# Kernel tuning notes

Measured on AMD Instinct MI355X. Metric: run time of the kernel, lower is better.

The kernel has to match this reference:

```python
import jax, jax.numpy as jnp
import numpy as np

B, H, S, D = 2, 16, 2048, 64
NEG = -1000000000.0


def setup_inputs() -> dict:
    key = jax.random.key(0)
    kq, kk, kv, km = jax.random.split(key, 4)
    query = jax.random.normal(kq, (B, H, S, D), dtype=jnp.float32)
    k = jax.random.normal(kk, (B, H, S, D), dtype=jnp.float32)
    value = jax.random.normal(kv, (B, H, S, D), dtype=jnp.float32)
    m = jax.random.randint(km, (B, 1, 1, S), 0, 2).astype(jnp.bool_)
    return {"query": query, "key": k, "value": value, "m": m}


def reference(query, key, value, m):
    # scaled dot-product attention; dropout is identity (eval / p effectively off for deterministic baseline)
    scale = 1.0 / jnp.sqrt(jnp.asarray(query.shape[-1], dtype=query.dtype))
    scores = jnp.einsum('bhqd,bhkd->bhqk', query, key) * scale  # [B,H,S,S]
    scores = jnp.where(m, jnp.asarray(NEG, dtype=scores.dtype), scores)
    p_attn = jax.nn.softmax(scores, axis=-1)
    return jnp.einsum('bhqk,bhkd->bhqd', p_attn, value)
```

## Files before the change

### kernel.cpp

```cpp
#include <hip/hip_runtime.h>
#include <hip/hip_bf16.h>

#define S_LEN 2048
#define DH 64
#define C1 0.18033688011112043f
#define MOFF -16.0f
#define MNEG -1.0e9f

typedef float f32x4 __attribute__((ext_vector_type(4)));
typedef short s16x8 __attribute__((ext_vector_type(8)));
typedef unsigned int u32x2 __attribute__((ext_vector_type(2)));

__device__ __forceinline__ ushort f2bf(float x) {
  union { __hip_bfloat16 b; ushort u; } v;
  v.b = __float2bfloat16(x);
  return v.u;
}
__device__ __forceinline__ unsigned int pack2(float lo, float hi) {
  return (unsigned int)f2bf(lo) | ((unsigned int)f2bf(hi) << 16);
}
__device__ __forceinline__ float fexp2(float x) {
#if __has_builtin(__builtin_amdgcn_exp2f)
  return __builtin_amdgcn_exp2f(x);
#else
  return exp2f(x);
#endif
}

__global__ __launch_bounds__(256) void prep_kernel(
    const float* __restrict__ K, const float* __restrict__ V,
    s16x8* __restrict__ dst, int n8,
    const unsigned char* __restrict__ mraw, float* __restrict__ maskp,
    int nmask) {
  const int i = blockIdx.x * 256 + threadIdx.x;
  const float* src = (i < n8) ? K : V;
  const int j = i & (n8 - 1);
  f32x4 x = ((const f32x4*)src)[2 * j];
  f32x4 y = ((const f32x4*)src)[2 * j + 1];
  s16x8 u;
  u[0] = (short)f2bf(x[0]); u[1] = (short)f2bf(x[1]);
  u[2] = (short)f2bf(x[2]); u[3] = (short)f2bf(x[3]);
  u[4] = (short)f2bf(y[0]); u[5] = (short)f2bf(y[1]);
  u[6] = (short)f2bf(y[2]); u[7] = (short)f2bf(y[3]);
  dst[i] = u;

  if (blockIdx.x < 8) {
    __shared__ int flag;
    if (threadIdx.x == 0) flag = 0;
    __syncthreads();
    int any = 0;
    for (int t = threadIdx.x; t < nmask; t += 256)
      if ((t & 3) != 0 && mraw[t] != 0) any = 1;
    if (any) atomicOr(&flag, 1);
    __syncthreads();
    const int u8 = flag;
    const int* mi = (const int*)mraw;
    const int per = nmask >> 3;
    const int base = blockIdx.x * per;
    for (int t = threadIdx.x; t < per; t += 256) {
      int v = u8 ? (int)mraw[base + t] : mi[base + t];
      maskp[base + t] = v ? MNEG : MOFF;
    }
  }
}

__device__ __forceinline__ void stage_k_tile8(const ushort* __restrict__ gK,
                                              ushort* ldsbuf, int wv, int lane) {
  const int rs = lane >> 3;
  const int r = 8 * wv + rs;
  const int c = lane & 7;
  const ushort* g = gK + r * 64 + 8 * (c ^ rs);
  ushort* l = ldsbuf + wv * 512;
  __builtin_amdgcn_global_load_lds((const __attribute__((address_space(1))) void*)g,
                                   (__attribute__((address_space(3))) void*)l,
                                   16, 0, 0);
}

__device__ __forceinline__ void write_vt4(ushort* vtbuf, int v_k0, int v_d0,
                                          u32x2 a, u32x2 b) {
  const int kc = v_k0 >> 3;
  const int ko = (2 * v_k0) & 15;
#pragma unroll
  for (int j = 0; j < 2; ++j) {
    unsigned lo = __builtin_amdgcn_perm(b[j], a[j], 0x05040100u);
    unsigned hi = __builtin_amdgcn_perm(b[j], a[j], 0x07060302u);
    const int d0 = v_d0 + 2 * j, d1 = d0 + 1;
    *(unsigned*)((char*)vtbuf + 128 * d0 + 16 * (kc ^ (d0 & 7)) + ko) = lo;
    *(unsigned*)((char*)vtbuf + 128 * d1 + 16 * (kc ^ (d1 & 7)) + ko) = hi;
  }
}

__global__ __launch_bounds__(512) void attn3_kernel(
    const float* __restrict__ Qf, const ushort* __restrict__ Kb,
    const ushort* __restrict__ Vb, const float* __restrict__ maskp,
    float* __restrict__ O) {
  __shared__ __align__(16) ushort lds_k[2][64 * 64];
  __shared__ __align__(16) ushort lds_vt[2][64 * 64];
  __shared__ __align__(16) ushort lds_p[8 * 16 * 64];

  const int wg = blockIdx.x;
  const int swz = (wg & 7) * 64 + (wg >> 3);
  const int bh = swz >> 4;
  const int qt = swz & 15;
  const int bb = bh >> 4;

  const float* Qbase = Qf + (size_t)bh * S_LEN * DH + (size_t)qt * 128 * DH;
  const ushort* Kbase = Kb + (size_t)bh * S_LEN * DH;
  const ushort* Vbase = Vb + (size_t)bh * S_LEN * DH;
  const float* mb = maskp + (size_t)bb * S_LEN;
  float* Ob = O + (size_t)bh * S_LEN * DH + (size_t)qt * 128 * DH;

  const int tid = threadIdx.x;
  const int lane = tid & 63;
  const int wv = tid >> 6;
  const int lj = lane & 15;
  const int lg = lane >> 4;
  const int r7 = lj & 7;

  s16x8 qf[2];
  {
    const float* qr = Qbase + (size_t)(wv * 16 + lj) * DH + 8 * lg;
#pragma unroll
    for (int c = 0; c < 2; ++c) {
      f32x4 a = *(const f32x4*)(qr + 32 * c);
      f32x4 b = *(const f32x4*)(qr + 32 * c + 4);
      s16x8 u;
      u[0] = (short)f2bf(a[0] * C1); u[1] = (short)f2bf(a[1] * C1);
      u[2] = (short)f2bf(a[2] * C1); u[3] = (short)f2bf(a[3] * C1);
      u[4] = (short)f2bf(b[0] * C1); u[5] = (short)f2bf(b[1] * C1);
      u[6] = (short)f2bf(b[2] * C1); u[7] = (short)f2bf(b[3] * C1);
      qf[c] = u;
    }
  }

  f32x4 oacc[4];
#pragma unroll
  for (int dt = 0; dt < 4; ++dt) oacc[dt] = (f32x4){0.f, 0.f, 0.f, 0.f};
  float ps_acc = 0.0f;

  char* pw = (char*)(lds_p + wv * 1024);
  int off_r[2], off_w[4];
#pragma unroll
  for (int c = 0; c < 2; ++c) off_r[c] = 128 * lj + 16 * ((lg + 4 * c) ^ r7);
#pragma unroll
  for (int t = 0; t < 4; ++t)
    off_w[t] = 128 * lj + 16 * ((2 * t + (lg >> 1)) ^ r7) + 8 * (lg & 1);

  const int v_k0 = 2 * (tid & 31);
  const int v_d0 = (tid >> 5) * 4;

  f32x4 mnA[4], mnB[4];
  u32x2 va = {0, 0}, vb = {0, 0};

#pragma unroll
  for (int t = 0; t < 4; ++t) mnA[t] = *(const f32x4*)(mb + 16 * t + 4 * lg);
  stage_k_tile8(Kbase, &lds_k[0][0], wv, lane);
  {
    const ushort* s0 = Vbase + (size_t)v_k0 * DH + v_d0;
    va = *(const u32x2*)s0;
    vb = *(const u32x2*)(s0 + DH);
    write_vt4(&lds_vt[0][0], v_k0, v_d0, va, vb);
  }
  __syncthreads();

  auto body = [&](int kv, int cb, f32x4 (&mnc)[4], f32x4 (&mnn)[4]) {
    const int nx = kv + 64;
    const bool has = nx < S_LEN;
    if (has) {
#pragma unroll
      for (int t = 0; t < 4; ++t)
        mnn[t] = *(const f32x4*)(mb + nx + 16 * t + 4 * lg);
      stage_k_tile8(Kbase + (size_t)nx * DH, &lds_k[cb ^ 1][0], wv, lane);
      const ushort* s0 = Vbase + (size_t)(nx + v_k0) * DH + v_d0;
      va = *(const u32x2*)s0;
      vb = *(const u32x2*)(s0 + DH);
    }

    f32x4 st[4];
#pragma unroll
    for (int t = 0; t < 4; ++t) st[t] = mnc[t];
    const char* kb = (const char*)&lds_k[cb][0];
    __builtin_amdgcn_s_setprio(1);
#pragma unroll
    for (int t = 0; t < 4; ++t) {
      s16x8 kf0 = *(const s16x8*)(kb + 2048 * t + off_r[0]);
      st[t] = __builtin_amdgcn_mfma_f32_16x16x32_bf16(kf0, qf[0], st[t], 0, 0, 0);
      s16x8 kf1 = *(const s16x8*)(kb + 2048 * t + off_r[1]);
      st[t] = __builtin_amdgcn_mfma_f32_16x16x32_bf16(kf1, qf[1], st[t], 0, 0, 0);
    }
    __builtin_amdgcn_s_setprio(0);

#pragma unroll
    for (int t = 0; t < 4; ++t) {
      float p0 = fexp2(st[t][0]);
      float p1 = fexp2(st[t][1]);
      float p2 = fexp2(st[t][2]);
      float p3 = fexp2(st[t][3]);
      ps_acc += (p0 + p1) + (p2 + p3);
      *(unsigned*)(pw + off_w[t]) = pack2(p0, p1);
      *(unsigned*)(pw + off_w[t] + 4) = pack2(p2, p3);
    }
    asm volatile("s_waitcnt lgkmcnt(0)" ::: "memory");
    __builtin_amdgcn_sched_barrier(0);

    const char* vtb = (const char*)&lds_vt[cb][0];
    __builtin_amdgcn_s_setprio(1);
#pragma unroll
    for (int c = 0; c < 2; ++c) {
      s16x8 pf = *(const s16x8*)(pw + off_r[c]);
#pragma unroll
      for (int dt = 0; dt < 4; ++dt) {
        s16x8 vf = *(const s16x8*)(vtb + 2048 * dt + off_r[c]);
        oacc[dt] = __builtin_amdgcn_mfma_f32_16x16x32_bf16(vf, pf, oacc[dt], 0, 0, 0);
      }
    }
    __builtin_amdgcn_s_setprio(0);

    if (has) write_vt4(&lds_vt[cb ^ 1][0], v_k0, v_d0, va, vb);
    __syncthreads();
  };

  for (int kv = 0; kv < S_LEN; kv += 128) {
    body(kv, 0, mnA, mnB);
    body(kv + 64, 1, mnB, mnA);
  }

  ps_acc += __shfl_xor(ps_acc, 16);
  ps_acc += __shfl_xor(ps_acc, 32);
  const float inv = 1.0f / ps_acc;

  float* orow = Ob + (size_t)(wv * 16 + lj) * DH;
#pragma unroll
  for (int dt = 0; dt < 4; ++dt) {
    f32x4 v = oacc[dt];
    v[0] *= inv; v[1] *= inv; v[2] *= inv; v[3] *= inv;
    *(f32x4*)(orow + 16 * dt + 4 * lg) = v;
  }
}

extern "C" void kernel_launch(void* const* d_in, const int* in_sizes, int n_in,
                              void* d_out, int out_size, void* d_ws, size_t ws_size,
                              hipStream_t stream) {
  const float* Q = (const float*)d_in[0];
  const float* K = (const float*)d_in[1];
  const float* V = (const float*)d_in[2];
  const unsigned char* M = (const unsigned char*)d_in[3];
  float* Obuf = (float*)d_out;
  const int nmask = in_sizes[3];

  const size_t nelem = (size_t)2 * 16 * S_LEN * DH;
  ushort* kvb = (ushort*)d_ws;
  float* maskp = (float*)((char*)d_ws + 2 * nelem * sizeof(ushort));
  const int n8 = (int)(nelem / 8);

  hipLaunchKernelGGL(prep_kernel, dim3(2 * n8 / 256), dim3(256), 0, stream,
                     K, V, (s16x8*)kvb, n8, M, maskp, nmask);
  hipLaunchKernelGGL(attn3_kernel, dim3(512), dim3(512), 0, stream,
                     Q, kvb, kvb + nelem, maskp, Obuf);
}
```

Measured before the change: 157.7 us.

## Split KV range across two workgroups, pass P via ds_bpermute, add combine kernel

Splits each query tile's key range into two halves handled by separate workgroups (1024 instead of 512), writing unnormalized partial outputs and row sums to workspace, then adds a combine kernel that sums and normalizes. The P matrix is now redistributed across lanes with ds_bpermute instead of a round trip through LDS, and the MFMA operand order is swapped to match. Mask values are loaded per tile instead of being double-buffered in registers. This aims for better CU occupancy and less LDS traffic, at the cost of an extra kernel launch and extra global memory writes and reads for the partials.

```diff
diff --git a/kernel.cpp b/kernel.cpp
--- a/kernel.cpp
+++ b/kernel.cpp
@@ -6,10 +6,12 @@
 #define C1 0.18033688011112043f
 #define MOFF -16.0f
 #define MNEG -1.0e9f
+#define NROWS (32 * S_LEN)
 
 typedef float f32x4 __attribute__((ext_vector_type(4)));
 typedef short s16x8 __attribute__((ext_vector_type(8)));
 typedef unsigned int u32x2 __attribute__((ext_vector_type(2)));
+typedef unsigned int u32x4 __attribute__((ext_vector_type(4)));
 
 __device__ __forceinline__ ushort f2bf(float x) {
   union { __hip_bfloat16 b; ushort u; } v;
@@ -90,25 +92,28 @@
   }
 }
 
-__global__ __launch_bounds__(512) void attn3_kernel(
+__global__ __launch_bounds__(512, 8) void attn4_kernel(
     const float* __restrict__ Qf, const ushort* __restrict__ Kb,
     const ushort* __restrict__ Vb, const float* __restrict__ maskp,
-    float* __restrict__ O) {
+    float* __restrict__ Odir, float* __restrict__ Opart,
+    float* __restrict__ lpart, int nsplit) {
   __shared__ __align__(16) ushort lds_k[2][64 * 64];
   __shared__ __align__(16) ushort lds_vt[2][64 * 64];
-  __shared__ __align__(16) ushort lds_p[8 * 16 * 64];
 
   const int wg = blockIdx.x;
-  const int swz = (wg & 7) * 64 + (wg >> 3);
-  const int bh = swz >> 4;
-  const int qt = swz & 15;
+  const int swz = (wg & 7) * (64 * nsplit) + (wg >> 3);
+  const int s = (nsplit == 2) ? (swz >> 9) : 0;
+  const int bhqt = swz & 511;
+  const int bh = bhqt >> 4;
+  const int qt = bhqt & 15;
   const int bb = bh >> 4;
+  const int ntiles = 32 / nsplit;
+  const int tile0 = s * ntiles;
 
   const float* Qbase = Qf + (size_t)bh * S_LEN * DH + (size_t)qt * 128 * DH;
   const ushort* Kbase = Kb + (size_t)bh * S_LEN * DH;
   const ushort* Vbase = Vb + (size_t)bh * S_LEN * DH;
   const float* mb = maskp + (size_t)bb * S_LEN;
-  float* Ob = O + (size_t)bh * S_LEN * DH + (size_t)qt * 128 * DH;
 
   const int tid = threadIdx.x;
   const int lane = tid & 63;
@@ -138,58 +143,52 @@
   for (int dt = 0; dt < 4; ++dt) oacc[dt] = (f32x4){0.f, 0.f, 0.f, 0.f};
   float ps_acc = 0.0f;
 
-  char* pw = (char*)(lds_p + wv * 1024);
-  int off_r[2], off_w[4];
-#pragma unroll
-  for (int c = 0; c < 2; ++c) off_r[c] = 128 * lj + 16 * ((lg + 4 * c) ^ r7);
-#pragma unroll
-  for (int t = 0; t < 4; ++t)
-    off_w[t] = 128 * lj + 16 * ((2 * t + (lg >> 1)) ^ r7) + 8 * (lg & 1);
+  const int off_r0 = 128 * lj + 16 * ((lg + 0) ^ r7);
+  const int off_r1 = 128 * lj + 16 * ((lg + 4) ^ r7);
+  const int a0 = 4 * (32 * (lg & 1) + lj);
+  const int a1 = a0 + 64;
+  const bool hi = (lane & 32) != 0;
 
   const int v_k0 = 2 * (tid & 31);
   const int v_d0 = (tid >> 5) * 4;
 
-  f32x4 mnA[4], mnB[4];
   u32x2 va = {0, 0}, vb = {0, 0};
 
-#pragma unroll
-  for (int t = 0; t < 4; ++t) mnA[t] = *(const f32x4*)(mb + 16 * t + 4 * lg);
-  stage_k_tile8(Kbase, &lds_k[0][0], wv, lane);
+  stage_k_tile8(Kbase + (size_t)tile0 * 64 * DH, &lds_k[0][0], wv, lane);
   {
-    const ushort* s0 = Vbase + (size_t)v_k0 * DH + v_d0;
+    const ushort* s0 = Vbase + ((size_t)tile0 * 64 + v_k0) * DH + v_d0;
     va = *(const u32x2*)s0;
     vb = *(const u32x2*)(s0 + DH);
     write_vt4(&lds_vt[0][0], v_k0, v_d0, va, vb);
   }
   __syncthreads();
 
-  auto body = [&](int kv, int cb, f32x4 (&mnc)[4], f32x4 (&mnn)[4]) {
-    const int nx = kv + 64;
-    const bool has = nx < S_LEN;
+  auto body = [&](int tl, int cb, bool has) {
+    const int kv = tl * 64;
     if (has) {
-#pragma unroll
-      for (int t = 0; t < 4; ++t)
-        mnn[t] = *(const f32x4*)(mb + nx + 16 * t + 4 * lg);
-      stage_k_tile8(Kbase + (size_t)nx * DH, &lds_k[cb ^ 1][0], wv, lane);
-      const ushort* s0 = Vbase + (size_t)(nx + v_k0) * DH + v_d0;
+      stage_k_tile8(Kbase + (size_t)(kv + 64) * DH, &lds_k[cb ^ 1][0], wv, lane);
+      const ushort* s0 = Vbase + (size_t)(kv + 64 + v_k0) * DH + v_d0;
       va = *(const u32x2*)s0;
       vb = *(const u32x2*)(s0 + DH);
     }
 
     f32x4 st[4];
 #pragma unroll
-    for (int t = 0; t < 4; ++t) st[t] = mnc[t];
+    for (int t = 0; t < 4; ++t)
+      st[t] = *(const f32x4*)(mb + kv + 16 * t + 4 * lg);
+
     const char* kb = (const char*)&lds_k[cb][0];
     __builtin_amdgcn_s_setprio(1);
 #pragma unroll
     for (int t = 0; t < 4; ++t) {
-      s16x8 kf0 = *(const s16x8*)(kb + 2048 * t + off_r[0]);
+      s16x8 kf0 = *(const s16x8*)(kb + 2048 * t + off_r0);
       st[t] = __builtin_amdgcn_mfma_f32_16x16x32_bf16(kf0, qf[0], st[t], 0, 0, 0);
-      s16x8 kf1 = *(const s16x8*)(kb + 2048 * t + off_r[1]);
+      s16x8 kf1 = *(const s16x8*)(kb + 2048 * t + off_r1);
       st[t] = __builtin_amdgcn_mfma_f32_16x16x32_bf16(kf1, qf[1], st[t], 0, 0, 0);
     }
     __builtin_amdgcn_s_setprio(0);
 
+    unsigned W[4], X[4];
 #pragma unroll
     for (int t = 0; t < 4; ++t) {
       float p0 = fexp2(st[t][0]);
@@ -197,21 +196,39 @@
       float p2 = fexp2(st[t][2]);
       float p3 = fexp2(st[t][3]);
       ps_acc += (p0 + p1) + (p2 + p3);
-      *(unsigned*)(pw + off_w[t]) = pack2(p0, p1);
-      *(unsigned*)(pw + off_w[t] + 4) = pack2(p2, p3);
-    }
-    asm volatile("s_waitcnt lgkmcnt(0)" ::: "memory");
-    __builtin_amdgcn_sched_barrier(0);
+      W[t] = pack2(p0, p1);
+      X[t] = pack2(p2, p3);
+    }
+
+    u32x4 pu[2];
+#pragma unroll
+    for (int c = 0; c < 2; ++c) {
+      const int tA = 2 * c, tB = 2 * c + 1;
+      unsigned w0 = (unsigned)__builtin_amdgcn_ds_bpermute(a0, (int)W[tA]);
+      unsigned w1 = (unsigned)__builtin_amdgcn_ds_bpermute(a0, (int)W[tB]);
+      unsigned x0 = (unsigned)__builtin_amdgcn_ds_bpermute(a0, (int)X[tA]);
+      unsigned x1 = (unsigned)__builtin_amdgcn_ds_bpermute(a0, (int)X[tB]);
+      unsigned w2 = (unsigned)__builtin_amdgcn_ds_bpermute(a1, (int)W[tA]);
+      unsigned w3 = (unsigned)__builtin_amdgcn_ds_bpermute(a1, (int)W[tB]);
+      unsigned x2 = (unsigned)__builtin_amdgcn_ds_bpermute(a1, (int)X[tA]);
+      unsigned x3 = (unsigned)__builtin_amdgcn_ds_bpermute(a1, (int)X[tB]);
+      pu[c][0] = hi ? w1 : w0;
+      pu[c][1] = hi ? x1 : x0;
+      pu[c][2] = hi ? w3 : w2;
+      pu[c][3] = hi ? x3 : x2;
+    }
 
     const char* vtb = (const char*)&lds_vt[cb][0];
     __builtin_amdgcn_s_setprio(1);
 #pragma unroll
     for (int c = 0; c < 2; ++c) {
-      s16x8 pf = *(const s16x8*)(pw + off_r[c]);
+      union { u32x4 u; s16x8 v; } pf;
+      pf.u = pu[c];
+      const int orc = c ? off_r1 : off_r0;
 #pragma unroll
       for (int dt = 0; dt < 4; ++dt) {
-        s16x8 vf = *(const s16x8*)(vtb + 2048 * dt + off_r[c]);
-        oacc[dt] = __builtin_amdgcn_mfma_f32_16x16x32_bf16(vf, pf, oacc[dt], 0, 0, 0);
+        s16x8 vf = *(const s16x8*)(vtb + 2048 * dt + orc);
+        oacc[dt] = __builtin_amdgcn_mfma_f32_16x16x32_bf16(pf.v, vf, oacc[dt], 0, 0, 0);
       }
     }
     __builtin_amdgcn_s_setprio(0);
@@ -220,22 +237,52 @@
     __syncthreads();
   };
 
-  for (int kv = 0; kv < S_LEN; kv += 128) {
-    body(kv, 0, mnA, mnB);
-    body(kv + 64, 1, mnB, mnA);
+  for (int i = 0; i < ntiles; i += 2) {
+    body(tile0 + i, 0, true);
+    body(tile0 + i + 1, 1, i + 2 < ntiles);
   }
 
   ps_acc += __shfl_xor(ps_acc, 16);
   ps_acc += __shfl_xor(ps_acc, 32);
-  const float inv = 1.0f / ps_acc;
-
-  float* orow = Ob + (size_t)(wv * 16 + lj) * DH;
-#pragma unroll
-  for (int dt = 0; dt < 4; ++dt) {
-    f32x4 v = oacc[dt];
-    v[0] *= inv; v[1] *= inv; v[2] *= inv; v[3] *= inv;
-    *(f32x4*)(orow + 16 * dt + 4 * lg) = v;
-  }
+
+  const int qrow0 = qt * 128 + wv * 16;
+  if (nsplit == 2) {
+    float* prow = Opart + ((size_t)s * NROWS + (size_t)bh * S_LEN + qrow0) * DH;
+#pragma unroll
+    for (int dt = 0; dt < 4; ++dt)
+#pragma unroll
+      for (int r = 0; r < 4; ++r)
+        prow[(4 * lg + r) * DH + 16 * dt + lj] = oacc[dt][r];
+    if (lg == 0)
+      lpart[(size_t)s * NROWS + (size_t)bh * S_LEN + qrow0 + lj] = ps_acc;
+  } else {
+    float invr[4];
+#pragma unroll
+    for (int r = 0; r < 4; ++r)
+      invr[r] = 1.0f / __shfl(ps_acc, 4 * lg + r);
+    float* orow = Odir + ((size_t)bh * S_LEN + qrow0) * DH;
+#pragma unroll
+    for (int dt = 0; dt < 4; ++dt)
+#pragma unroll
+      for (int r = 0; r < 4; ++r)
+        orow[(4 * lg + r) * DH + 16 * dt + lj] = oacc[dt][r] * invr[r];
+  }
+}
+
+__global__ __launch_bounds__(256) void combine_kernel(
+    const float* __restrict__ Op, const float* __restrict__ lp,
+    float* __restrict__ O) {
+  const int g = blockIdx.x * 256 + threadIdx.x;
+  const int row = g >> 4;
+  const float inv = 1.0f / (lp[row] + lp[NROWS + row]);
+  f32x4 a = ((const f32x4*)Op)[g];
+  f32x4 b = ((const f32x4*)(Op + (size_t)NROWS * DH))[g];
+  f32x4 o;
+  o[0] = (a[0] + b[0]) * inv;
+  o[1] = (a[1] + b[1]) * inv;
+  o[2] = (a[2] + b[2]) * inv;
+  o[3] = (a[3] + b[3]) * inv;
+  ((f32x4*)O)[g] = o;
 }
 
 extern "C" void kernel_launch(void* const* d_in, const int* in_sizes, int n_in,
@@ -249,12 +296,30 @@
   const int nmask = in_sizes[3];
 
   const size_t nelem = (size_t)2 * 16 * S_LEN * DH;
+  const size_t kv_bytes = 2 * nelem * sizeof(ushort);
+  const size_t maskp_off = kv_bytes;
+  const size_t opart_off = kv_bytes + (64 << 10);
+  const size_t opart_bytes = (size_t)2 * NROWS * DH * 4;
+  const size_t lp_off = opart_off + opart_bytes;
+  const size_t need2 = lp_off + (size_t)2 * NROWS * 4;
+
   ushort* kvb = (ushort*)d_ws;
-  float* maskp = (float*)((char*)d_ws + 2 * nelem * sizeof(ushort));
+  float* maskp = (float*)((char*)d_ws + maskp_off);
   const int n8 = (int)(nelem / 8);
 
   hipLaunchKernelGGL(prep_kernel, dim3(2 * n8 / 256), dim3(256), 0, stream,
                      K, V, (s16x8*)kvb, n8, M, maskp, nmask);
-  hipLaunchKernelGGL(attn3_kernel, dim3(512), dim3(512), 0, stream,
-                     Q, kvb, kvb + nelem, maskp, Obuf);
-}
+
+  if (ws_size >= need2) {
+    float* Opart = (float*)((char*)d_ws + opart_off);
+    float* lpart = (float*)((char*)d_ws + lp_off);
+    hipLaunchKernelGGL(attn4_kernel, dim3(1024), dim3(512), 0, stream,
+                       Q, kvb, kvb + nelem, maskp, Obuf, Opart, lpart, 2);
+    hipLaunchKernelGGL(combine_kernel, dim3(NROWS * DH / 4 / 256), dim3(256), 0,
+                       stream, Opart, lpart, Obuf);
+  } else {
+    hipLaunchKernelGGL(attn4_kernel, dim3(512), dim3(512), 0, stream,
+                       Q, kvb, kvb + nelem, maskp, Obuf, (float*)d_ws,
+                       (float*)d_ws, 1);
+  }
+}
```

Measured after the change: 315.9 us. 100% more time.
